# Kernel tuning notes

Measured on AMD Instinct MI355X. Metric: run time of the kernel, lower is better.

Reference implementation:

```python
import jax, jax.numpy as jnp
import numpy as np

B, T, D = 64, 512, 1536   # batch, time, enc_size (2*768)
H = 30                    # z_rnn_size
L_SUP, R_SUP = -0.1, 1.1  # HardKuma stretched support
EPS = 1e-5


def setup_inputs() -> dict:
    key = jax.random.key(0)
    ks = jax.random.split(key, 12)
    s = 0.02
    return {
        "x": jax.random.normal(ks[0], (B, T, D), dtype=jnp.float32),
        "u": jax.random.uniform(ks[1], (B, T, 1), dtype=jnp.float32),
        # LSTMCell(enc_size + 1 -> H), torch gate order [i, f, g, o]
        "Wih": jax.random.normal(ks[2], (4 * H, D + 1), dtype=jnp.float32) * s,
        "Whh": jax.random.normal(ks[3], (4 * H, H), dtype=jnp.float32) * s,
        "bih": jax.random.normal(ks[4], (4 * H,), dtype=jnp.float32) * s,
        "bhh": jax.random.normal(ks[5], (4 * H,), dtype=jnp.float32) * s,
        # KumaGate: Linear(D + H -> 1) + Softplus for a and b
        "Wa": jax.random.normal(ks[6], (1, D + H), dtype=jnp.float32) * s,
        "ba": jax.random.normal(ks[7], (1,), dtype=jnp.float32) * s,
        "Wb": jax.random.normal(ks[8], (1, D + H), dtype=jnp.float32) * s,
        "bb": jax.random.normal(ks[9], (1,), dtype=jnp.float32) * s,
    }


def reference(x, u, Wih, Whh, bih, bhh, Wa, ba, Wb, bb):
    # x: [B, T, D], u: [B, T, 1] uniform reparam noise
    hseq = jnp.swapaxes(x, 0, 1)               # [T, B, D]
    useq = jnp.swapaxes(u, 0, 1)               # [T, B, 1]
    batch = x.shape[0]

    def step(carry, inp):
        hx, cx = carry                          # [B, H] each
        h_t, u_t = inp                          # [B, D], [B, 1]
        feat = jnp.concatenate([h_t, hx], axis=-1)          # [B, D+H]
        a = jnp.clip(jax.nn.softplus(feat @ Wa.T + ba), 1e-6, 100.0)
        b = jnp.clip(jax.nn.softplus(feat @ Wb.T + bb), 1e-6, 100.0)
        # HardKuma reparameterized sample (training branch)
        uu = jnp.clip(u_t, EPS, 1.0 - EPS)
        s = (1.0 - (1.0 - uu) ** (1.0 / b)) ** (1.0 / a)     # Kuma icdf
        t = s * (R_SUP - L_SUP) + L_SUP                      # stretch
        z_t = jnp.clip(t, 0.0, 1.0)                          # hard rectify, [B, 1]
        # LSTMCell update (torch gate order i, f, g, o)
        rnn_in = jnp.concatenate([h_t, z_t], axis=-1)        # [B, D+1]
        gates = rnn_in @ Wih.T + bih + hx @ Whh.T + bhh      # [B, 4H]
        i, f, g, o = jnp.split(gates, 4, axis=-1)
        c_new = jax.nn.sigmoid(f) * cx + jax.nn.sigmoid(i) * jnp.tanh(g)
        h_new = jax.nn.sigmoid(o) * jnp.tanh(c_new)
        return (h_new, c_new), z_t

    init = (jnp.zeros((batch, H), x.dtype), jnp.zeros((batch, H), x.dtype))
    _, zs = jax.lax.scan(step, init, (hseq, useq))           # zs: [T, B, 1]
    return jnp.swapaxes(zs[..., 0], 0, 1)                    # [B, T]
```

## Files before the change

### kernel.cpp

```cpp
#include <hip/hip_runtime.h>
#include <math.h>

#define Bb 64
#define Tt 512
#define Dd 1536
#define Hh 30
#define NC 128
#define Mm (Bb*Tt)
#define KC 32
#define XSTR 72
#define WSTR 132

__device__ __forceinline__ float rcpf_(float x) { return __builtin_amdgcn_rcpf(x); }
__device__ __forceinline__ float sigmoidf_(float x) {
    return rcpf_(1.f + __expf(-x));
}
__device__ __forceinline__ float tanhf_fast(float x) {
    float e = __expf(2.f * x);
    return fmaf(-2.f, rcpf_(e + 1.f), 1.f);
}
__device__ __forceinline__ float softplus_(float x) {
    return fmaxf(x, 0.f) + __logf(1.f + __expf(-fabsf(x)));
}
__device__ __forceinline__ float rl_f(float v, int lane) {
    return __uint_as_float(__builtin_amdgcn_readlane(__float_as_uint(v), lane));
}

__global__ __launch_bounds__(256) void pack_w(const float* __restrict__ Wih,
                                              const float* __restrict__ Wa,
                                              const float* __restrict__ Wb,
                                              float* __restrict__ Wp) {
    int idx = blockIdx.x * 256 + threadIdx.x;
    int k = idx >> 7;
    int c = idx & 127;
    float v = 0.f;
    if (c < 120)       v = Wih[c * (Dd + 1) + k];
    else if (c == 120) v = Wa[k];
    else if (c == 121) v = Wb[k];
    Wp[idx] = v;
}

__global__ __launch_bounds__(256) void pack_s(const float* __restrict__ Wih,
                                              const float* __restrict__ Whh,
                                              const float* __restrict__ Wa,
                                              const float* __restrict__ Wb,
                                              float* __restrict__ WAp,
                                              float* __restrict__ WBp) {
    int t = threadIdx.x;
    for (int idx = t; idx < 64 * 32; idx += 256) {
        int l = idx >> 5, k = idx & 31;
        float va = 0.f, vb = 0.f;
        if (k < 30) {
            if (l < 30)                 { va = Whh[l * Hh + k];        vb = Whh[(30 + l) * Hh + k]; }
            else if (l == 30)           { va = Wa[Dd + k]; }
            else if (l == 31)           { va = Wb[Dd + k]; }
            else if (l < 62)            { va = Whh[(l + 28) * Hh + k]; vb = Whh[(l + 58) * Hh + k]; }
        } else if (k == 30) {
            if (l < 30)                 { va = Wih[l * (Dd + 1) + Dd];        vb = Wih[(30 + l) * (Dd + 1) + Dd]; }
            else if (l >= 32 && l < 62) { va = Wih[(l + 28) * (Dd + 1) + Dd]; vb = Wih[(l + 58) * (Dd + 1) + Dd]; }
        }
        WAp[idx] = va;
        WBp[idx] = vb;
    }
}

__global__ __launch_bounds__(256, 2) void gemm_k(const float* __restrict__ X,
                                                 const float* __restrict__ Wp,
                                                 const float* __restrict__ bih,
                                                 const float* __restrict__ bhh,
                                                 const float* __restrict__ ba,
                                                 const float* __restrict__ bbp,
                                                 float* __restrict__ GX) {
    __shared__ float Xs[KC][XSTR];
    __shared__ float Ws[KC][WSTR];
    const int t  = threadIdx.x;
    const int m0 = blockIdx.x * 64;
    const int tc = t & 15;
    const int tr = t >> 4;
    const int c0 = tc * 8;
    const int r0 = tr * 4;

    float acc[4][8];
#pragma unroll
    for (int r = 0; r < 4; r++)
#pragma unroll
        for (int c = 0; c < 8; c++) acc[r][c] = 0.f;

    const int xr = t >> 3;
    const int kk = (t & 7) * 4;
    const int kw = t >> 3;
    const int cw = (t & 7) * 16;

    for (int k0 = 0; k0 < Dd; k0 += KC) {
        {
            const float4 xv0 = *(const float4*)(X + (size_t)(m0 + xr) * Dd + k0 + kk);
            const float4 xv1 = *(const float4*)(X + (size_t)(m0 + xr + 32) * Dd + k0 + kk);
            Xs[kk + 0][xr] = xv0.x;  Xs[kk + 1][xr] = xv0.y;
            Xs[kk + 2][xr] = xv0.z;  Xs[kk + 3][xr] = xv0.w;
            Xs[kk + 0][xr + 32] = xv1.x;  Xs[kk + 1][xr + 32] = xv1.y;
            Xs[kk + 2][xr + 32] = xv1.z;  Xs[kk + 3][xr + 32] = xv1.w;
        }
        {
            const float* src = Wp + (size_t)(k0 + kw) * NC + cw;
#pragma unroll
            for (int i = 0; i < 4; i++) {
                *(float4*)&Ws[kw][cw + 4 * i] = *(const float4*)(src + 4 * i);
            }
        }
        __syncthreads();
#pragma unroll 8
        for (int k = 0; k < KC; k++) {
            float4 xf  = *(const float4*)&Xs[k][r0];
            float4 wf0 = *(const float4*)&Ws[k][c0];
            float4 wf1 = *(const float4*)&Ws[k][c0 + 4];
            float xr4[4] = {xf.x, xf.y, xf.z, xf.w};
            float wc[8]  = {wf0.x, wf0.y, wf0.z, wf0.w, wf1.x, wf1.y, wf1.z, wf1.w};
#pragma unroll
            for (int r = 0; r < 4; r++)
#pragma unroll
                for (int c = 0; c < 8; c++)
                    acc[r][c] = fmaf(xr4[r], wc[c], acc[r][c]);
        }
        __syncthreads();
    }

    float biasv[8];
#pragma unroll
    for (int c = 0; c < 8; c++) {
        int cc = c0 + c;
        biasv[c] = (cc < 120) ? (bih[cc] + bhh[cc])
                 : (cc == 120) ? ba[0]
                 : (cc == 121) ? bbp[0] : 0.f;
    }
#pragma unroll
    for (int r = 0; r < 4; r++) {
        float4 o0, o1;
        o0.x = acc[r][0] + biasv[0]; o0.y = acc[r][1] + biasv[1];
        o0.z = acc[r][2] + biasv[2]; o0.w = acc[r][3] + biasv[3];
        o1.x = acc[r][4] + biasv[4]; o1.y = acc[r][5] + biasv[5];
        o1.z = acc[r][6] + biasv[6]; o1.w = acc[r][7] + biasv[7];
        float* dst = GX + (size_t)(m0 + r0 + r) * NC + c0;
        *(float4*)(dst + 0) = o0;
        *(float4*)(dst + 4) = o1;
    }
}

#define PIN16(A, B) asm volatile("" \
    : "+v"(A[B+0]), "+v"(A[B+1]), "+v"(A[B+2]),  "+v"(A[B+3]),  "+v"(A[B+4]),  "+v"(A[B+5]),  "+v"(A[B+6]),  "+v"(A[B+7]), \
      "+v"(A[B+8]), "+v"(A[B+9]), "+v"(A[B+10]), "+v"(A[B+11]), "+v"(A[B+12]), "+v"(A[B+13]), "+v"(A[B+14]), "+v"(A[B+15]))

__global__
__attribute__((amdgpu_flat_work_group_size(64, 64)))
__attribute__((amdgpu_waves_per_eu(1)))
void scan_k(const float* __restrict__ u,
            const float* __restrict__ gx,
            const float* __restrict__ WAp,
            const float* __restrict__ WBp,
            float* __restrict__ out) {
    __shared__ float lus[Tt];
    __shared__ float zbuf[Tt];
    const int b = blockIdx.x;
    const int l = threadIdx.x;

    for (int k = l; k < Tt; k += 64) {
        float uu = u[b * Tt + k];
        uu = fminf(fmaxf(uu, 1e-5f), 1.f - 1e-5f);
        lus[k] = __logf(1.f - uu);
    }
    __syncthreads();

    float wA[32], wB[32];
#pragma unroll
    for (int j = 0; j < 8; j++) {
        float4 a4 = ((const float4*)(WAp + l * 32))[j];
        float4 b4 = ((const float4*)(WBp + l * 32))[j];
        wA[4 * j + 0] = a4.x; wA[4 * j + 1] = a4.y; wA[4 * j + 2] = a4.z; wA[4 * j + 3] = a4.w;
        wB[4 * j + 0] = b4.x; wB[4 * j + 1] = b4.y; wB[4 * j + 2] = b4.z; wB[4 * j + 3] = b4.w;
    }

    int cA, cB;
    if (l < 30)       { cA = l;       cB = 30 + l; }
    else if (l == 30) { cA = 120;     cB = 122; }
    else if (l == 31) { cA = 121;     cB = 123; }
    else if (l < 62)  { cA = l + 28;  cB = l + 58; }
    else              { cA = 126;     cB = 127; }
    const float* gxb = gx + (size_t)b * Tt * NC;

    float h[Hh];
#pragma unroll
    for (int k = 0; k < Hh; k++) h[k] = 0.f;
    float cst = 0.f;

    float gA0 = gxb[cA], gB0 = gxb[cB];
    float gA1 = gxb[NC + cA], gB1 = gxb[NC + cB];
    float lu0 = lus[0], lu1 = lus[1];

    const int srcb = ((l & 31) + 32) << 2;

    for (int t = 0; t < Tt; t++) {
        PIN16(wA, 0); PIN16(wA, 16);
        PIN16(wB, 0); PIN16(wB, 16);

        float a0 = gA0, a1 = 0.f, a2 = 0.f, a3 = 0.f;
        float b0 = gB0, b1 = 0.f, b2 = 0.f, b3 = 0.f;
#pragma unroll
        for (int k = 0; k < 28; k += 4) {
            a0 = fmaf(wA[k], h[k], a0);         a1 = fmaf(wA[k + 1], h[k + 1], a1);
            a2 = fmaf(wA[k + 2], h[k + 2], a2); a3 = fmaf(wA[k + 3], h[k + 3], a3);
            b0 = fmaf(wB[k], h[k], b0);         b1 = fmaf(wB[k + 1], h[k + 1], b1);
            b2 = fmaf(wB[k + 2], h[k + 2], b2); b3 = fmaf(wB[k + 3], h[k + 3], b3);
        }
        a0 = fmaf(wA[28], h[28], a0); a1 = fmaf(wA[29], h[29], a1);
        b0 = fmaf(wB[28], h[28], b0); b1 = fmaf(wB[29], h[29], b1);
        float accA = (a0 + a2) + (a1 + a3);
        float accB = (b0 + b2) + (b1 + b3);

        gA0 = gA1; gB0 = gB1;
        float lu = lu0; lu0 = lu1;
        if (t + 2 < Tt) {
            gA1 = gxb[(size_t)(t + 2) * NC + cA];
            gB1 = gxb[(size_t)(t + 2) * NC + cB];
            lu1 = lus[t + 2];
        }

        const float av = rl_f(accA, 30);
        const float bv = rl_f(accA, 31);
        float a  = fminf(fmaxf(softplus_(av), 1e-6f), 100.f);
        float bk = fminf(fmaxf(softplus_(bv), 1e-6f), 100.f);
        float p = __expf(lu * rcpf_(bk));
        float inner = 1.f - p;
        float s = (inner <= 0.f) ? 0.f : __expf(__logf(inner) * rcpf_(a));
        float z = fminf(fmaxf(fmaf(1.2f, s, -0.1f), 0.f), 1.f);

        accA = fmaf(z, wA[30], accA);
        accB = fmaf(z, wB[30], accB);

        const float tg = tanhf_fast(accA);
        const float sA = sigmoidf_(accA);
        const float sB = sigmoidf_(accB);
        const float gg_t = __uint_as_float(__builtin_amdgcn_ds_bpermute(srcb, __float_as_uint(tg)));
        const float oo_s = __uint_as_float(__builtin_amdgcn_ds_bpermute(srcb, __float_as_uint(sB)));

        const float cn = fmaf(sB, cst, sA * gg_t);
        const float hn = oo_s * tanhf_fast(cn);
        cst = cn;
#pragma unroll
        for (int k = 0; k < Hh; k++) h[k] = rl_f(hn, k);
        if (l == 0) zbuf[t] = z;
    }
    __syncthreads();
    for (int k = l; k < Tt; k += 64) out[b * Tt + k] = zbuf[k];
}

extern "C" void kernel_launch(void* const* d_in, const int* in_sizes, int n_in,
                              void* d_out, int out_size, void* d_ws, size_t ws_size,
                              hipStream_t stream) {
    const float* x   = (const float*)d_in[0];
    const float* u   = (const float*)d_in[1];
    const float* Wih = (const float*)d_in[2];
    const float* Whh = (const float*)d_in[3];
    const float* bih = (const float*)d_in[4];
    const float* bhh = (const float*)d_in[5];
    const float* Wa  = (const float*)d_in[6];
    const float* ba  = (const float*)d_in[7];
    const float* Wb  = (const float*)d_in[8];
    const float* bbp = (const float*)d_in[9];
    float* out = (float*)d_out;

    char* wsb = (char*)d_ws;
    float* Wp  = (float*)(wsb);
    float* WAp = (float*)(wsb + 786432);
    float* WBp = (float*)(wsb + 794624);
    float* GX  = (float*)(wsb + 802816);

    pack_w<<<(Dd * NC) / 256, 256, 0, stream>>>(Wih, Wa, Wb, Wp);
    pack_s<<<1, 256, 0, stream>>>(Wih, Whh, Wa, Wb, WAp, WBp);
    gemm_k<<<Mm / 64, 256, 0, stream>>>(x, Wp, bih, bhh, ba, bbp, GX);
    scan_k<<<Bb, 64, 0, stream>>>(u, GX, WAp, WBp, out);
}
```

Baseline: 810.5 us.

## Replace FP32 SIMT input GEMM with split-bf16 MFMA (3-term) GEMM

```diff
diff --git a/kernel.cpp b/kernel.cpp
--- a/kernel.cpp
+++ b/kernel.cpp
@@ -7,9 +7,11 @@
 #define Hh 30
 #define NC 128
 #define Mm (Bb*Tt)
-#define KC 32
-#define XSTR 72
-#define WSTR 132
+#define KSTEPS 48
+
+typedef unsigned short u16;
+typedef __attribute__((ext_vector_type(8))) short short8v;
+typedef __attribute__((ext_vector_type(4))) float f32x4;
 
 __device__ __forceinline__ float rcpf_(float x) { return __builtin_amdgcn_rcpf(x); }
 __device__ __forceinline__ float sigmoidf_(float x) {
@@ -26,18 +28,47 @@
     return __uint_as_float(__builtin_amdgcn_readlane(__float_as_uint(v), lane));
 }
 
+__device__ __forceinline__ f32x4 mm_bf16(short8v a, short8v b, f32x4 c) {
+    return __builtin_amdgcn_mfma_f32_16x16x32_bf16(a, b, c, 0, 0, 0);
+}
+
+union U4S8 { unsigned int u[4]; short8v s; };
+
+__device__ __forceinline__ void cvt_split(const float4 a, const float4 b,
+                                          short8v& hi, short8v& lo) {
+    float x[8] = {a.x, a.y, a.z, a.w, b.x, b.y, b.z, b.w};
+    U4S8 H, L;
+#pragma unroll
+    for (int i = 0; i < 4; i++) {
+        unsigned int u0 = __float_as_uint(x[2 * i]);
+        unsigned int u1 = __float_as_uint(x[2 * i + 1]);
+        unsigned int h0 = u0 & 0xffff0000u;
+        unsigned int h1 = u1 & 0xffff0000u;
+        H.u[i] = (u0 >> 16) | h1;
+        float l0 = x[2 * i]     - __uint_as_float(h0);
+        float l1 = x[2 * i + 1] - __uint_as_float(h1);
+        L.u[i] = (__float_as_uint(l0) >> 16) | (__float_as_uint(l1) & 0xffff0000u);
+    }
+    hi = H.s;
+    lo = L.s;
+}
+
 __global__ __launch_bounds__(256) void pack_w(const float* __restrict__ Wih,
                                               const float* __restrict__ Wa,
                                               const float* __restrict__ Wb,
-                                              float* __restrict__ Wp) {
-    int idx = blockIdx.x * 256 + threadIdx.x;
-    int k = idx >> 7;
-    int c = idx & 127;
+                                              u16* __restrict__ Wbh,
+                                              u16* __restrict__ Wbl) {
+    const int k = blockIdx.x * 256 + threadIdx.x;
+    const int c = blockIdx.y;
     float v = 0.f;
     if (c < 120)       v = Wih[c * (Dd + 1) + k];
     else if (c == 120) v = Wa[k];
     else if (c == 121) v = Wb[k];
-    Wp[idx] = v;
+    unsigned int u = __float_as_uint(v);
+    unsigned int h = u & 0xffff0000u;
+    float lo = v - __uint_as_float(h);
+    Wbh[(size_t)c * Dd + k] = (u16)(u >> 16);
+    Wbl[(size_t)c * Dd + k] = (u16)(__float_as_uint(lo) >> 16);
 }
 
 __global__ __launch_bounds__(256) void pack_s(const float* __restrict__ Wih,
@@ -65,84 +96,111 @@
 }
 
 __global__ __launch_bounds__(256, 2) void gemm_k(const float* __restrict__ X,
-                                                 const float* __restrict__ Wp,
+                                                 const u16* __restrict__ Wbh,
+                                                 const u16* __restrict__ Wbl,
                                                  const float* __restrict__ bih,
                                                  const float* __restrict__ bhh,
                                                  const float* __restrict__ ba,
                                                  const float* __restrict__ bbp,
                                                  float* __restrict__ GX) {
-    __shared__ float Xs[KC][XSTR];
-    __shared__ float Ws[KC][WSTR];
-    const int t  = threadIdx.x;
-    const int m0 = blockIdx.x * 64;
-    const int tc = t & 15;
-    const int tr = t >> 4;
-    const int c0 = tc * 8;
-    const int r0 = tr * 4;
-
-    float acc[4][8];
-#pragma unroll
-    for (int r = 0; r < 4; r++)
-#pragma unroll
-        for (int c = 0; c < 8; c++) acc[r][c] = 0.f;
-
-    const int xr = t >> 3;
-    const int kk = (t & 7) * 4;
-    const int kw = t >> 3;
-    const int cw = (t & 7) * 16;
-
-    for (int k0 = 0; k0 < Dd; k0 += KC) {
-        {
-            const float4 xv0 = *(const float4*)(X + (size_t)(m0 + xr) * Dd + k0 + kk);
-            const float4 xv1 = *(const float4*)(X + (size_t)(m0 + xr + 32) * Dd + k0 + kk);
-            Xs[kk + 0][xr] = xv0.x;  Xs[kk + 1][xr] = xv0.y;
-            Xs[kk + 2][xr] = xv0.z;  Xs[kk + 3][xr] = xv0.w;
-            Xs[kk + 0][xr + 32] = xv1.x;  Xs[kk + 1][xr + 32] = xv1.y;
-            Xs[kk + 2][xr + 32] = xv1.z;  Xs[kk + 3][xr + 32] = xv1.w;
+    const int t    = threadIdx.x;
+    const int lane = t & 63;
+    const int wid  = t >> 6;
+    const int wrow = wid >> 1;
+    const int wcol = wid & 1;
+    const int m0   = blockIdx.x * 64 + wrow * 32;
+    const int n0   = wcol * 64;
+    const int lr   = lane & 15;
+    const int lk   = lane >> 4;
+
+    const float* xa0 = X + (size_t)(m0 + lr) * Dd + lk * 8;
+    const float* xa1 = xa0 + (size_t)16 * Dd;
+    const u16*   pbh = Wbh + (size_t)(n0 + lr) * Dd + lk * 8;
+    const u16*   pbl = Wbl + (size_t)(n0 + lr) * Dd + lk * 8;
+
+    f32x4 acc[2][4];
+#pragma unroll
+    for (int nt = 0; nt < 4; nt++) {
+        int c = n0 + nt * 16 + lr;
+        float bv = (c < 120) ? (bih[c] + bhh[c])
+                 : (c == 120) ? ba[0]
+                 : (c == 121) ? bbp[0] : 0.f;
+        f32x4 v = {bv, bv, bv, bv};
+        acc[0][nt] = v;
+        acc[1][nt] = v;
+    }
+
+#define LOADA(ra, ks) do {                                        \
+        ra[0] = *(const float4*)(xa0 + (ks) * 32);                \
+        ra[1] = *(const float4*)(xa0 + (ks) * 32 + 4);            \
+        ra[2] = *(const float4*)(xa1 + (ks) * 32);                \
+        ra[3] = *(const float4*)(xa1 + (ks) * 32 + 4);            \
+    } while (0)
+
+#define LOADB(bh, bl, ks) do {                                               \
+        _Pragma("unroll")                                                    \
+        for (int nt = 0; nt < 4; nt++) {                                     \
+            bh[nt] = *(const short8v*)(pbh + (size_t)nt * 16 * Dd + (ks) * 32); \
+            bl[nt] = *(const short8v*)(pbl + (size_t)nt * 16 * Dd + (ks) * 32); \
+        }                                                                    \
+    } while (0)
+
+#define STEP(ra, bh, bl) do {                                     \
+        short8v ah0, al0, ah1, al1;                               \
+        cvt_split(ra[0], ra[1], ah0, al0);                        \
+        cvt_split(ra[2], ra[3], ah1, al1);                        \
+        _Pragma("unroll")                                         \
+        for (int nt = 0; nt < 4; nt++)                            \
+            acc[0][nt] = mm_bf16(ah0, bh[nt], acc[0][nt]);        \
+        _Pragma("unroll")                                         \
+        for (int nt = 0; nt < 4; nt++)                            \
+            acc[1][nt] = mm_bf16(ah1, bh[nt], acc[1][nt]);        \
+        _Pragma("unroll")                                         \
+        for (int nt = 0; nt < 4; nt++)                            \
+            acc[0][nt] = mm_bf16(al0, bh[nt], acc[0][nt]);        \
+        _Pragma("unroll")                                         \
+        for (int nt = 0; nt < 4; nt++)                            \
+            acc[1][nt] = mm_bf16(al1, bh[nt], acc[1][nt]);        \
+        _Pragma("unroll")                                         \
+        for (int nt = 0; nt < 4; nt++)                            \
+            acc[0][nt] = mm_bf16(ah0, bl[nt], acc[0][nt]);        \
+        _Pragma("unroll")                                         \
+        for (int nt = 0; nt < 4; nt++)                            \
+            acc[1][nt] = mm_bf16(ah1, bl[nt], acc[1][nt]);        \
+    } while (0)
+
+    float4  ra0[4], ra1[4];
+    short8v bh0[4], bl0[4], bh1[4], bl1[4];
+
+    LOADA(ra0, 0);
+    LOADB(bh0, bl0, 0);
+    int ks = 0;
+    for (; ks < KSTEPS - 2; ks += 2) {
+        LOADA(ra1, ks + 1);
+        LOADB(bh1, bl1, ks + 1);
+        STEP(ra0, bh0, bl0);
+        LOADA(ra0, ks + 2);
+        LOADB(bh0, bl0, ks + 2);
+        STEP(ra1, bh1, bl1);
+    }
+    LOADA(ra1, KSTEPS - 1);
+    LOADB(bh1, bl1, KSTEPS - 1);
+    STEP(ra0, bh0, bl0);
+    STEP(ra1, bh1, bl1);
+
+#undef LOADA
+#undef LOADB
+#undef STEP
+
+#pragma unroll
+    for (int mt = 0; mt < 2; mt++)
+#pragma unroll
+        for (int nt = 0; nt < 4; nt++) {
+            float* dst = GX + (size_t)(m0 + mt * 16 + lk * 4) * NC + n0 + nt * 16 + lr;
+#pragma unroll
+            for (int r = 0; r < 4; r++)
+                dst[(size_t)r * NC] = acc[mt][nt][r];
         }
-        {
-            const float* src = Wp + (size_t)(k0 + kw) * NC + cw;
-#pragma unroll
-            for (int i = 0; i < 4; i++) {
-                *(float4*)&Ws[kw][cw + 4 * i] = *(const float4*)(src + 4 * i);
-            }
-        }
-        __syncthreads();
-#pragma unroll 8
-        for (int k = 0; k < KC; k++) {
-            float4 xf  = *(const float4*)&Xs[k][r0];
-            float4 wf0 = *(const float4*)&Ws[k][c0];
-            float4 wf1 = *(const float4*)&Ws[k][c0 + 4];
-            float xr4[4] = {xf.x, xf.y, xf.z, xf.w};
-            float wc[8]  = {wf0.x, wf0.y, wf0.z, wf0.w, wf1.x, wf1.y, wf1.z, wf1.w};
-#pragma unroll
-            for (int r = 0; r < 4; r++)
-#pragma unroll
-                for (int c = 0; c < 8; c++)
-                    acc[r][c] = fmaf(xr4[r], wc[c], acc[r][c]);
-        }
-        __syncthreads();
-    }
-
-    float biasv[8];
-#pragma unroll
-    for (int c = 0; c < 8; c++) {
-        int cc = c0 + c;
-        biasv[c] = (cc < 120) ? (bih[cc] + bhh[cc])
-                 : (cc == 120) ? ba[0]
-                 : (cc == 121) ? bbp[0] : 0.f;
-    }
-#pragma unroll
-    for (int r = 0; r < 4; r++) {
-        float4 o0, o1;
-        o0.x = acc[r][0] + biasv[0]; o0.y = acc[r][1] + biasv[1];
-        o0.z = acc[r][2] + biasv[2]; o0.w = acc[r][3] + biasv[3];
-        o1.x = acc[r][4] + biasv[4]; o1.y = acc[r][5] + biasv[5];
-        o1.z = acc[r][6] + biasv[6]; o1.w = acc[r][7] + biasv[7];
-        float* dst = GX + (size_t)(m0 + r0 + r) * NC + c0;
-        *(float4*)(dst + 0) = o0;
-        *(float4*)(dst + 4) = o1;
-    }
 }
 
 #define PIN16(A, B) asm volatile("" \
@@ -268,13 +326,14 @@
     float* out = (float*)d_out;
 
     char* wsb = (char*)d_ws;
-    float* Wp  = (float*)(wsb);
+    u16*   Wbh = (u16*)(wsb);
+    u16*   Wbl = (u16*)(wsb + 393216);
     float* WAp = (float*)(wsb + 786432);
     float* WBp = (float*)(wsb + 794624);
     float* GX  = (float*)(wsb + 802816);
 
-    pack_w<<<(Dd * NC) / 256, 256, 0, stream>>>(Wih, Wa, Wb, Wp);
+    pack_w<<<dim3(Dd / 256, NC), 256, 0, stream>>>(Wih, Wa, Wb, Wbh, Wbl);
     pack_s<<<1, 256, 0, stream>>>(Wih, Whh, Wa, Wb, WAp, WBp);
-    gemm_k<<<Mm / 64, 256, 0, stream>>>(x, Wp, bih, bhh, ba, bbp, GX);
+    gemm_k<<<Mm / 64, 256, 0, stream>>>(x, Wbh, Wbl, bih, bhh, ba, bbp, GX);
     scan_k<<<Bb, 64, 0, stream>>>(u, GX, WAp, WBp, out);
 }
```

Measured after the change: 782.6 us. 3.4% less time.
